# Kernel optimization log

Measured on AMD Instinct MI355X. Metric: run time of the kernel, lower is better.

## Reference

```python
import jax, jax.numpy as jnp
import numpy as np

B, P, K, G_PER, F_IN, H, NECK = 16, 512, 32, 8, 59, 128, 512
N = B * P
E = N * K
G = N // G_PER
EPS = 1e-5


def setup_inputs() -> dict:
    rng = np.random.default_rng(0)
    f32 = lambda a: jnp.asarray(a, jnp.float32)
    x = f32(rng.standard_normal((N, F_IN)))
    pos = f32(rng.standard_normal((N, 3)) * 8.0)
    nrm = rng.standard_normal((N, 3))
    normal = f32(nrm / np.linalg.norm(nrm, axis=1, keepdims=True))
    # synthetic radius-graph edges: K neighbors per node within its own graph, incl. self edge
    nbr = rng.integers(0, P, size=(N, K))
    nbr[:, 0] = np.arange(N) % P  # self edge guarantees every dst segment is non-empty
    starts = np.repeat(np.arange(B) * P, P)
    src = jnp.asarray((starts[:, None] + nbr).reshape(-1), jnp.int32)
    dst = jnp.asarray(np.repeat(np.arange(N), K), jnp.int32)
    # raw (unnormalized but consecutive-run) residue labels, relabeled inside reference
    pool_batch = jnp.asarray(np.repeat(np.arange(G) * 3 + 7, G_PER), jnp.int32)
    mask_t = f32(np.repeat(rng.integers(0, 2, size=G), G_PER))
    def lin(i, o, bias=True):
        w = f32(rng.standard_normal((i, o)) / np.sqrt(i))
        return (w, f32(np.zeros(o))) if bias else w
    lin_w, lin_b = lin(F_IN, H)
    src_w = lin(F_IN, H, bias=False)
    dst_w = lin(F_IN, H, bias=False)
    posnn_w, posnn_b = lin(6, H)
    attnn_w, attnn_b = lin(H, H)
    neck_w, neck_b = lin(H, NECK)
    mlp1_w, mlp1_b = lin(NECK, 256)
    mlp2_w, mlp2_b = lin(256, 1)
    gb = lambda n: (f32(1.0 + 0.1 * rng.standard_normal(n)), f32(0.1 * rng.standard_normal(n)))
    posnn_g, posnn_bb = gb(H)
    attnn_g, attnn_bb = gb(H)
    neck_g, neck_bb = gb(NECK)
    mlp1_g, mlp1_bb = gb(256)
    return dict(x=x, pos=pos, normal=normal, mask_t=mask_t, pool_batch=pool_batch,
                src=src, dst=dst, lin_w=lin_w, lin_b=lin_b, src_w=src_w, dst_w=dst_w,
                posnn_w=posnn_w, posnn_b=posnn_b, posnn_g=posnn_g, posnn_bb=posnn_bb,
                attnn_w=attnn_w, attnn_b=attnn_b, attnn_g=attnn_g, attnn_bb=attnn_bb,
                neck_w=neck_w, neck_b=neck_b, neck_g=neck_g, neck_bb=neck_bb,
                mlp1_w=mlp1_w, mlp1_b=mlp1_b, mlp1_g=mlp1_g, mlp1_bb=mlp1_bb,
                mlp2_w=mlp2_w, mlp2_b=mlp2_b)


def bn_relu(h, g, b):
    # eval-mode BatchNorm1d (running_mean=0, running_var=1) + ReLU; Dropout is identity in eval
    return jax.nn.relu(h * (g / jnp.sqrt(1.0 + EPS)) + b)


def reference(x, pos, normal, mask_t, pool_batch, src, dst,
              lin_w, lin_b, src_w, dst_w,
              posnn_w, posnn_b, posnn_g, posnn_bb,
              attnn_w, attnn_b, attnn_g, attnn_bb,
              neck_w, neck_b, neck_g, neck_bb,
              mlp1_w, mlp1_b, mlp1_g, mlp1_bb,
              mlp2_w, mlp2_b):
    n = x.shape[0]
    # vectorized form of the per-element relabel loop: consecutive runs -> 0..G-1
    chg = jnp.concatenate([jnp.zeros((1,), jnp.int32),
                           (pool_batch[1:] != pool_batch[:-1]).astype(jnp.int32)])
    pb = jnp.cumsum(chg)
    # --- PointTransformerConv (gather -> pos_nn/attn_nn MLPs -> segment softmax -> scatter-add)
    v = x @ lin_w + lin_b                      # value projection [N,H]
    a_src = (x @ src_w)[src]                   # lin_src(x_j)   [E,H]
    a_dst = (x @ dst_w)[dst]                   # lin_dst(x_i)   [E,H]
    rel = jnp.concatenate([pos[dst] - pos[src], normal[dst] - normal[src]], axis=-1)  # [E,6]
    delta = bn_relu(rel @ posnn_w + posnn_b, posnn_g, posnn_bb)                       # [E,H]
    alpha = bn_relu((a_dst - a_src + delta) @ attnn_w + attnn_b, attnn_g, attnn_bb)   # [E,H]
    amax = jax.ops.segment_max(alpha, dst, num_segments=n)
    e = jnp.exp(alpha - amax[dst])
    den = jax.ops.segment_sum(e, dst, num_segments=n)
    attn = e / (den[dst] + 1e-16)              # per-destination softmax over neighbors
    h = jax.ops.segment_sum(attn * (v[src] + delta), dst, num_segments=n)  # [N,H]
    # --- neck, residue max-pool, head
    h = bn_relu(h @ neck_w + neck_b, neck_g, neck_bb)          # [N,512]
    gfeat = jax.ops.segment_max(h, pb, num_segments=G)         # global_max_pool  [G,512]
    gfeat = bn_relu(gfeat @ mlp1_w + mlp1_b, mlp1_g, mlp1_bb)  # [G,256]
    out = gfeat @ mlp2_w + mlp2_b                              # [G,1]
    mask_g = jax.ops.segment_max(mask_t, pb, num_segments=G)   # pooled mask_t
    # original does out[mask_t]; we zero non-selected rows to keep shapes static
    return out * (mask_g == 1.0).astype(out.dtype)[:, None]
```

## Files before the change

### kernel.cpp

```cpp
#include <hip/hip_runtime.h>
#include <hip/hip_bf16.h>
#include <cmath>

#define N_NODES 8192
#define F_INPUT 59
#define H 128
#define K 32
#define NECK 512
#define GPER 8
#define NG 1024
#define EPS_BN 1e-5f
#define LOG2E 1.44269504088896340736f
#define DPITCH 136
#define XPITCH 72
#define PLANE 272

typedef short bf16x8 __attribute__((ext_vector_type(8)));
typedef float f32x16 __attribute__((ext_vector_type(16)));

__device__ __forceinline__ void split_bf(float v, short& hi, short& lo) {
    unsigned u = __float_as_uint(v);
    float hif = __uint_as_float(u & 0xffff0000u);
    hi = (short)(u >> 16);
    lo = (short)(__float_as_uint(v - hif) >> 16);
}
__device__ __forceinline__ short f2bfrn(float f) {
    __hip_bfloat16 b = __float2bfloat16(f);
    return *reinterpret_cast<short*>(&b);
}

__device__ __forceinline__ int bfrag_idx(int k, int c, int k16) {
    int ct = c >> 5, ln = c & 31;
    int s = k >> 4, hf = (k >> 3) & 1, kk = k & 7;
    return ((((ct * k16 + s) * 2 + hf) * 32 + ln) * 8 + kk);
}

__global__ __launch_bounds__(256) void prep_kernel(
    const float* __restrict__ lin_w,
    const float* __restrict__ src_w, const float* __restrict__ dst_w,
    const float* __restrict__ posnn_w,
    const float* __restrict__ attnn_w, const float* __restrict__ attnn_g,
    const float* __restrict__ neck_w,
    short* __restrict__ w3hi, short* __restrict__ w3lo,
    short* __restrict__ pwhi, short* __restrict__ pwlo,
    short* __restrict__ awhi, short* __restrict__ awlo,
    short* __restrict__ nwhi, short* __restrict__ nwlo)
{
    const int b = blockIdx.x;
    if (b < F_INPUT) {
        const int c = threadIdx.x;
        if (c < H) {
            float a1 = 0.f, a2 = 0.f;
            for (int k = 0; k < H; k++) {
                float wa = attnn_w[k * H + c];
                a1 = fmaf(src_w[b * H + k], wa, a1);
                a2 = fmaf(dst_w[b * H + k], wa, a2);
            }
            short hi, lo; int idx;
            split_bf(lin_w[b * H + c], hi, lo);
            idx = bfrag_idx(b, c, 4);       w3hi[idx] = hi; w3lo[idx] = lo;
            split_bf(a1, hi, lo);
            idx = bfrag_idx(b, 128 + c, 4); w3hi[idx] = hi; w3lo[idx] = lo;
            split_bf(a2, hi, lo);
            idx = bfrag_idx(b, 256 + c, 4); w3hi[idx] = hi; w3lo[idx] = lo;
        }
    } else if (b == F_INPUT) {
        for (int t = threadIdx.x; t < 5 * 384; t += 256) {
            int k = F_INPUT + t / 384, c = t % 384;
            int idx = bfrag_idx(k, c, 4);
            w3hi[idx] = 0; w3lo[idx] = 0;
        }
    } else if (b == F_INPUT + 1) {
        for (int idx = threadIdx.x; idx < 2048; idx += 256) {
            int kk = idx & 7; int t = idx >> 3;
            int l2 = t & 31; t >>= 5;
            int hb = t & 1;  t >>= 1;
            int ct = t;
            int k = hb * 8 + kk, c = ct * 32 + l2;
            float wv = (k < 6) ? posnn_w[k * H + c] : 0.f;
            short hi, lo; split_bf(wv, hi, lo);
            pwhi[idx] = hi; pwlo[idx] = lo;
        }
    } else if (b < F_INPUT + 2 + 64) {
        int idx = (b - F_INPUT - 2) * 256 + threadIdx.x;
        int kk = idx & 7; int t = idx >> 3;
        int l2 = t & 31; t >>= 5;
        int hb = t & 1;  t >>= 1;
        int s  = t & 7;  t >>= 3;
        int c = t * 32 + l2, k = s * 16 + hb * 8 + kk;
        float scale = attnn_g[c] * rsqrtf(1.f + EPS_BN) * LOG2E;
        short hi, lo; split_bf(attnn_w[k * H + c] * scale, hi, lo);
        awhi[idx] = hi; awlo[idx] = lo;
    } else {
        int idx = (b - F_INPUT - 2 - 64) * 256 + threadIdx.x;
        int kk = idx & 7; int t = idx >> 3;
        int l2 = t & 31; t >>= 5;
        int hb = t & 1;  t >>= 1;
        int s  = t & 7;  t >>= 3;
        int c = t * 32 + l2, k = s * 16 + hb * 8 + kk;
        short hi, lo; split_bf(neck_w[k * NECK + c], hi, lo);
        nwhi[idx] = hi; nwlo[idx] = lo;
    }
}

__global__ __launch_bounds__(256) void proj_kernel(
    const float* __restrict__ x, const float* __restrict__ lin_b,
    const float* __restrict__ attnn_g, const float* __restrict__ attnn_b,
    const float* __restrict__ attnn_bb,
    const short* __restrict__ w3hi, const short* __restrict__ w3lo,
    float2* __restrict__ vx, float* __restrict__ xdb)
{
    const int n0 = blockIdx.x * 32;
    const int tid = threadIdx.x;
    const int wave = tid >> 6;
    const int lane = tid & 63;
    const int hf = lane >> 5;
    const int ln = lane & 31;

    __shared__ __align__(16) short xhi[32][XPITCH];
    __shared__ __align__(16) short xlo[32][XPITCH];

    for (int idx = tid; idx < 32 * F_INPUT; idx += 256) {
        int n = idx / F_INPUT, k = idx - n * F_INPUT;
        short hi, lo; split_bf(x[n0 * F_INPUT + idx], hi, lo);
        xhi[n][k] = hi; xlo[n][k] = lo;
    }
    if (tid < 32 * 5) {
        int n = tid / 5, k = F_INPUT + tid % 5;
        xhi[n][k] = 0; xlo[n][k] = 0;
    }
    __syncthreads();

    f32x16 acc[3];
    #pragma unroll
    for (int t = 0; t < 3; t++)
        #pragma unroll
        for (int r = 0; r < 16; r++) acc[t][r] = 0.f;

    #pragma unroll
    for (int s = 0; s < 4; s++) {
        bf16x8 ah = *(const bf16x8*)&xhi[ln][s * 16 + hf * 8];
        bf16x8 al = *(const bf16x8*)&xlo[ln][s * 16 + hf * 8];
        #pragma unroll
        for (int t = 0; t < 3; t++) {
            const int ct = wave + 4 * t;
            const int boff = (((ct * 4 + s) * 2 + hf) * 32 + ln) * 8;
            bf16x8 bh = *(const bf16x8*)&w3hi[boff];
            bf16x8 bl = *(const bf16x8*)&w3lo[boff];
            acc[t] = __builtin_amdgcn_mfma_f32_32x32x16_bf16(ah, bl, acc[t], 0, 0, 0);
            acc[t] = __builtin_amdgcn_mfma_f32_32x32x16_bf16(al, bh, acc[t], 0, 0, 0);
            acc[t] = __builtin_amdgcn_mfma_f32_32x32x16_bf16(ah, bh, acc[t], 0, 0, 0);
        }
    }
    const int c = wave * 32 + ln;
    const float lb  = lin_b[c];
    const float s0  = attnn_g[c] * rsqrtf(1.f + EPS_BN);
    const float as_ = s0 * LOG2E;
    const float cbn = fmaf(attnn_b[c], s0, attnn_bb[c]) * LOG2E;
    #pragma unroll
    for (int r = 0; r < 16; r++) {
        int node = n0 + (r & 3) + 8 * (r >> 2) + 4 * hf;
        vx[node * H + c] = make_float2(as_ * acc[1][r], acc[0][r] + lb);
        xdb[node * H + c] = fmaf(acc[2][r], as_, cbn);
    }
}

__global__ __launch_bounds__(256) void edge_kernel(
    const float* __restrict__ pos, const float* __restrict__ normal,
    const int* __restrict__ src,
    const float2* __restrict__ vx, const float* __restrict__ xdb,
    const float* __restrict__ posnn_b, const float* __restrict__ posnn_g,
    const float* __restrict__ posnn_bb,
    const short* __restrict__ pwhi, const short* __restrict__ pwlo,
    const short* __restrict__ awhi, const short* __restrict__ awlo,
    unsigned* __restrict__ h2)
{
    const int i0 = blockIdx.x * 2;
    const int tid = threadIdx.x;
    const int wave = tid >> 6;
    const int lane = tid & 63;
    const int hf = lane >> 5;
    const int ln = lane & 31;

    __shared__ int srcs[2][K];
    __shared__ __align__(16) short dpk[32 * PLANE];

    const int cc = wave * 32 + ln;
    const float ps  = posnn_g[cc] * rsqrtf(1.f + EPS_BN);
    const float pbn = fmaf(posnn_b[cc], ps, posnn_bb[cc]);

    const bf16x8 pbh = *(const bf16x8*)&pwhi[((wave * 2 + hf) * 32 + ln) * 8];
    const bf16x8 pbl = *(const bf16x8*)&pwlo[((wave * 2 + hf) * 32 + ln) * 8];

    bf16x8 rah[2], ral[2];
    #pragma unroll
    for (int n = 0; n < 2; n++)
        #pragma unroll
        for (int k = 0; k < 8; k++) { rah[n][k] = 0; ral[n][k] = 0; }
    if (hf == 0) {
        #pragma unroll
        for (int n = 0; n < 2; n++) {
            const int i = i0 + n;
            int s = src[i * K + ln];
            if (wave == 0) srcs[n][ln] = s * H;
            short h_, l_;
            #pragma unroll
            for (int k = 0; k < 3; k++) {
                split_bf(pos[i * 3 + k] - pos[s * 3 + k], h_, l_);
                rah[n][k] = h_; ral[n][k] = l_;
                split_bf(normal[i * 3 + k] - normal[s * 3 + k], h_, l_);
                rah[n][k + 3] = h_; ral[n][k + 3] = l_;
            }
        }
    }

    const int dbase = ((cc >> 4) * 2 + ((cc >> 3) & 1)) * PLANE + (cc & 7);

    float dreg[2][16];
    #pragma unroll
    for (int n = 0; n < 2; n++) {
        f32x16 da;
        #pragma unroll
        for (int r = 0; r < 16; r++) da[r] = 0.f;
        da = __builtin_amdgcn_mfma_f32_32x32x16_bf16(rah[n], pbl, da, 0, 0, 0);
        da = __builtin_amdgcn_mfma_f32_32x32x16_bf16(ral[n], pbh, da, 0, 0, 0);
        da = __builtin_amdgcn_mfma_f32_32x32x16_bf16(rah[n], pbh, da, 0, 0, 0);
        #pragma unroll
        for (int r = 0; r < 16; r++) {
            int j = (r & 3) + 8 * (r >> 2) + 4 * hf;
            float d = fmaxf(fmaf(da[r], ps, pbn), 0.f);
            dreg[n][r] = d;
            dpk[n * 16 * PLANE + dbase + j * 8] = f2bfrn(d);
        }
    }
    __syncthreads();

    const short* whb = awhi + wave * 8 * 2 * 32 * 8;
    const short* wlb = awlo + wave * 8 * 2 * 32 * 8;

    #pragma unroll
    for (int n = 0; n < 2; n++) {
        const int i = i0 + n;
        f32x16 acc;
        #pragma unroll
        for (int r = 0; r < 16; r++) acc[r] = 0.f;
        #pragma unroll
        for (int s = 0; s < 8; s++) {
            bf16x8 ah = *(const bf16x8*)&dpk[((n * 8 + s) * 2 + hf) * PLANE + ln * 8];
            const int boff = ((s * 2 + hf) * 32 + ln) * 8;
            bf16x8 bh = *(const bf16x8*)&whb[boff];
            bf16x8 bl = *(const bf16x8*)&wlb[boff];
            acc = __builtin_amdgcn_mfma_f32_32x32x16_bf16(ah, bh, acc, 0, 0, 0);
            acc = __builtin_amdgcn_mfma_f32_32x32x16_bf16(ah, bl, acc, 0, 0, 0);
        }

        const float base = xdb[i * H + cc];
        float e[16];
        float den = 0.f;
        #pragma unroll
        for (int r = 0; r < 16; r++) {
            int j = (r & 3) + 8 * (r >> 2) + 4 * hf;
            float2 g = vx[srcs[n][j] + cc];
            float av = fmaxf(acc[r] + base - g.x, 0.f);
            float ev = exp2f(av);
            e[r] = ev;
            den += ev;
            dreg[n][r] += g.y;
        }
        den += __shfl_xor(den, 32, 64);
        const float inv = 1.f / (den + 1e-16f);

        float hsum = 0.f;
        #pragma unroll
        for (int r = 0; r < 16; r++)
            hsum = fmaf(e[r], dreg[n][r], hsum);
        hsum += __shfl_xor(hsum, 32, 64);
        hsum *= inv;
        if (hf == 0) {
            unsigned u = __float_as_uint(hsum);
            unsigned hib = u & 0xffff0000u;
            unsigned lo = __float_as_uint(hsum - __uint_as_float(hib)) >> 16;
            h2[i * H + cc] = (lo << 16) | (u >> 16);
        }
    }
}

__global__ __launch_bounds__(256) void neck_head_kernel(
    const unsigned* __restrict__ h2,
    const short* __restrict__ nwhi, const short* __restrict__ nwlo,
    const float* __restrict__ neck_b, const float* __restrict__ neck_g,
    const float* __restrict__ neck_bb,
    const float* __restrict__ mask_t,
    const float* __restrict__ mlp1_w, const float* __restrict__ mlp1_b,
    const float* __restrict__ mlp1_g, const float* __restrict__ mlp1_bb,
    const float* __restrict__ mlp2_w, const float* __restrict__ mlp2_b,
    float* __restrict__ out)
{
    const int blk = blockIdx.x;
    const int n0 = blk * 32;
    const int tid = threadIdx.x;
    const int wave = tid >> 6;
    const int lane = tid & 63;
    const int hf = lane >> 5;
    const int ln = lane & 31;

    __shared__ __align__(16) short a_hi[32][DPITCH];
    __shared__ __align__(16) short a_lo[32][DPITCH];
    __shared__ float gfeat_l[4][NECK];
    __shared__ float red_l[4][4][256];

    for (int d = tid; d < 32 * H; d += 256) {
        unsigned u = h2[(n0 + (d >> 7)) * H + (d & 127)];
        a_hi[d >> 7][d & 127] = (short)(u & 0xffffu);
        a_lo[d >> 7][d & 127] = (short)(u >> 16);
    }
    __syncthreads();

    f32x16 acc[4];
    #pragma unroll
    for (int t = 0; t < 4; t++)
        #pragma unroll
        for (int r = 0; r < 16; r++) acc[t][r] = 0.f;

    #pragma unroll
    for (int s = 0; s < 8; s++) {
        bf16x8 ah = *(const bf16x8*)&a_hi[ln][s * 16 + hf * 8];
        bf16x8 al = *(const bf16x8*)&a_lo[ln][s * 16 + hf * 8];
        #pragma unroll
        for (int t = 0; t < 4; t++) {
            const int ct = wave * 4 + t;
            const int boff = (((ct * 8 + s) * 2 + hf) * 32 + ln) * 8;
            bf16x8 bh = *(const bf16x8*)&nwhi[boff];
            bf16x8 bl = *(const bf16x8*)&nwlo[boff];
            acc[t] = __builtin_amdgcn_mfma_f32_32x32x16_bf16(ah, bl, acc[t], 0, 0, 0);
            acc[t] = __builtin_amdgcn_mfma_f32_32x32x16_bf16(al, bh, acc[t], 0, 0, 0);
            acc[t] = __builtin_amdgcn_mfma_f32_32x32x16_bf16(ah, bh, acc[t], 0, 0, 0);
        }
    }

    #pragma unroll
    for (int t = 0; t < 4; t++) {
        const int c = wave * 128 + t * 32 + ln;
        const float s  = neck_g[c] * rsqrtf(1.f + EPS_BN);
        const float bnb = fmaf(neck_b[c], s, neck_bb[c]);
        #pragma unroll
        for (int g = 0; g < 4; g++) {
            float m = 0.f;
            #pragma unroll
            for (int q = 0; q < 4; q++)
                m = fmaxf(m, fmaf(acc[t][4 * g + q], s, bnb));
            m = fmaxf(m, __shfl_xor(m, 32, 64));
            if (hf == 0) gfeat_l[g][c] = m;
        }
    }
    __syncthreads();

    const int c4 = lane;
    float ph[4][4];
    #pragma unroll
    for (int g = 0; g < 4; g++)
        #pragma unroll
        for (int mm = 0; mm < 4; mm++) ph[g][mm] = 0.f;

    const int k0 = wave * 128;
    for (int k = 0; k < 128; k += 4) {
        float4 gv[4];
        #pragma unroll
        for (int g = 0; g < 4; g++) gv[g] = *(const float4*)&gfeat_l[g][k0 + k];
        #pragma unroll
        for (int kk = 0; kk < 4; kk++) {
            float w0 = mlp1_w[(k0 + k + kk) * 256 + c4];
            float w1 = mlp1_w[(k0 + k + kk) * 256 + c4 + 64];
            float w2 = mlp1_w[(k0 + k + kk) * 256 + c4 + 128];
            float w3 = mlp1_w[(k0 + k + kk) * 256 + c4 + 192];
            #pragma unroll
            for (int g = 0; g < 4; g++) {
                float gvk = (&gv[g].x)[kk];
                ph[g][0] = fmaf(gvk, w0, ph[g][0]);
                ph[g][1] = fmaf(gvk, w1, ph[g][1]);
                ph[g][2] = fmaf(gvk, w2, ph[g][2]);
                ph[g][3] = fmaf(gvk, w3, ph[g][3]);
            }
        }
    }
    #pragma unroll
    for (int g = 0; g < 4; g++)
        #pragma unroll
        for (int mm = 0; mm < 4; mm++)
            red_l[wave][g][c4 + 64 * mm] = ph[g][mm];
    __syncthreads();

    {
        const int g = wave;
        float part = 0.f;
        #pragma unroll
        for (int mm = 0; mm < 4; mm++) {
            const int c = c4 + 64 * mm;
            float sum = mlp1_b[c] + red_l[0][g][c] + red_l[1][g][c]
                      + red_l[2][g][c] + red_l[3][g][c];
            float s = mlp1_g[c] * rsqrtf(1.f + EPS_BN);
            float val = fmaxf(fmaf(sum, s, mlp1_bb[c]), 0.f);
            part = fmaf(val, mlp2_w[c], part);
        }
        #pragma unroll
        for (int off = 32; off > 0; off >>= 1) part += __shfl_xor(part, off, 64);
        if (lane == 0) {
            const int gg = blk * 4 + g;
            float mm = mask_t[gg * GPER];
            #pragma unroll
            for (int n = 1; n < GPER; n++) mm = fmaxf(mm, mask_t[gg * GPER + n]);
            out[gg] = (mm == 1.0f) ? (part + mlp2_b[0]) : 0.f;
        }
    }
}

extern "C" void kernel_launch(void* const* d_in, const int* in_sizes, int n_in,
                              void* d_out, int out_size, void* d_ws, size_t ws_size,
                              hipStream_t stream)
{
    const float* x        = (const float*)d_in[0];
    const float* pos      = (const float*)d_in[1];
    const float* normal   = (const float*)d_in[2];
    const float* mask_t   = (const float*)d_in[3];
    const int*   src      = (const int*)d_in[5];
    const float* lin_w    = (const float*)d_in[7];
    const float* lin_b    = (const float*)d_in[8];
    const float* src_w    = (const float*)d_in[9];
    const float* dst_w    = (const float*)d_in[10];
    const float* posnn_w  = (const float*)d_in[11];
    const float* posnn_b  = (const float*)d_in[12];
    const float* posnn_g  = (const float*)d_in[13];
    const float* posnn_bb = (const float*)d_in[14];
    const float* attnn_w  = (const float*)d_in[15];
    const float* attnn_b  = (const float*)d_in[16];
    const float* attnn_g  = (const float*)d_in[17];
    const float* attnn_bb = (const float*)d_in[18];
    const float* neck_w   = (const float*)d_in[19];
    const float* neck_b   = (const float*)d_in[20];
    const float* neck_g   = (const float*)d_in[21];
    const float* neck_bb  = (const float*)d_in[22];
    const float* mlp1_w   = (const float*)d_in[23];
    const float* mlp1_b   = (const float*)d_in[24];
    const float* mlp1_g   = (const float*)d_in[25];
    const float* mlp1_bb  = (const float*)d_in[26];
    const float* mlp2_w   = (const float*)d_in[27];
    const float* mlp2_b   = (const float*)d_in[28];

    float* ws = (float*)d_ws;
    float2*   vx   = (float2*)ws;
    float*    xdb  = (float*)(vx + (size_t)N_NODES * H);
    unsigned* h2   = (unsigned*)(xdb + (size_t)N_NODES * H);
    short*    w3hi = (short*)(h2 + (size_t)N_NODES * H);
    short*    w3lo = w3hi + 24576;
    short*    pwhi = w3lo + 24576;
    short*    pwlo = pwhi + 2048;
    short*    awhi = pwlo + 2048;
    short*    awlo = awhi + H * H;
    short*    nwhi = awlo + H * H;
    short*    nwlo = nwhi + H * NECK;

    prep_kernel<<<F_INPUT + 2 + 64 + 256, 256, 0, stream>>>(
        lin_w, src_w, dst_w, posnn_w, attnn_w, attnn_g, neck_w,
        w3hi, w3lo, pwhi, pwlo, awhi, awlo, nwhi, nwlo);
    proj_kernel<<<N_NODES / 32, 256, 0, stream>>>(x, lin_b, attnn_g, attnn_b, attnn_bb,
                                                  w3hi, w3lo, vx, xdb);
    edge_kernel<<<N_NODES / 2, 256, 0, stream>>>(pos, normal, src, vx, xdb,
                                                 posnn_b, posnn_g, posnn_bb,
                                                 pwhi, pwlo, awhi, awlo, h2);
    neck_head_kernel<<<N_NODES / 32, 256, 0, stream>>>(
        h2, nwhi, nwlo, neck_b, neck_g, neck_bb, mask_t,
        mlp1_w, mlp1_b, mlp1_g, mlp1_bb, mlp2_w, mlp2_b, (float*)d_out);
}
```

Baseline: 208.3 us.

## Software-pipeline edge kernel over 8 node pairs with double-buffered LDS

Each edge_kernel block now handles 16 nodes (8 pairs) instead of 2. The pos-MLP delta phase for the next pair is computed into a second LDS buffer while the attention epilogue of the current pair reads the first. This aims to overlap gather latency and MFMA work across pairs and to amortise per-block weight and BN-parameter loads. In exchange, LDS use doubles and register pressure rises, and the grid drops to 512 blocks, which may lower occupancy and load balance.

New measurement: 266.2 us. 1.28x slower.

```diff
diff --git a/kernel.cpp b/kernel.cpp
--- a/kernel.cpp
+++ b/kernel.cpp
@@ -165,6 +165,96 @@
     }
 }
 
+
+#define DELTA_PHASE(PAIR, DPKBUF, SRCSBUF, DREG)                                 \
+{                                                                                \
+    const int ii0 = n_base + (PAIR) * 2;                                         \
+    bf16x8 rah[2], ral[2];                                                       \
+    _Pragma("unroll")                                                            \
+    for (int n = 0; n < 2; n++)                                                  \
+        _Pragma("unroll")                                                        \
+        for (int k = 0; k < 8; k++) { rah[n][k] = 0; ral[n][k] = 0; }            \
+    if (hf == 0) {                                                               \
+        _Pragma("unroll")                                                        \
+        for (int n = 0; n < 2; n++) {                                            \
+            const int i = ii0 + n;                                               \
+            int s = src[i * K + ln];                                             \
+            if (wave == 0) SRCSBUF[n][ln] = s * H;                               \
+            short h_, l_;                                                        \
+            _Pragma("unroll")                                                    \
+            for (int k = 0; k < 3; k++) {                                        \
+                split_bf(pos[i * 3 + k] - pos[s * 3 + k], h_, l_);               \
+                rah[n][k] = h_; ral[n][k] = l_;                                  \
+                split_bf(normal[i * 3 + k] - normal[s * 3 + k], h_, l_);         \
+                rah[n][k + 3] = h_; ral[n][k + 3] = l_;                          \
+            }                                                                    \
+        }                                                                        \
+    }                                                                            \
+    _Pragma("unroll")                                                            \
+    for (int n = 0; n < 2; n++) {                                                \
+        f32x16 da;                                                               \
+        _Pragma("unroll")                                                        \
+        for (int r = 0; r < 16; r++) da[r] = 0.f;                                \
+        da = __builtin_amdgcn_mfma_f32_32x32x16_bf16(rah[n], pbl, da, 0, 0, 0);  \
+        da = __builtin_amdgcn_mfma_f32_32x32x16_bf16(ral[n], pbh, da, 0, 0, 0);  \
+        da = __builtin_amdgcn_mfma_f32_32x32x16_bf16(rah[n], pbh, da, 0, 0, 0);  \
+        _Pragma("unroll")                                                        \
+        for (int r = 0; r < 16; r++) {                                           \
+            int j = (r & 3) + 8 * (r >> 2) + 4 * hf;                             \
+            float d = fmaxf(fmaf(da[r], ps, pbn), 0.f);                          \
+            DREG[n][r] = d;                                                      \
+            DPKBUF[n * 16 * PLANE + dbase + j * 8] = f2bfrn(d);                  \
+        }                                                                        \
+    }                                                                            \
+}
+
+#define EPILOGUE_PHASE(PAIR, DPKBUF, SRCSBUF, DREG)                              \
+{                                                                                \
+    _Pragma("unroll")                                                            \
+    for (int n = 0; n < 2; n++) {                                                \
+        const int i = n_base + (PAIR) * 2 + n;                                   \
+        f32x16 acc;                                                              \
+        _Pragma("unroll")                                                        \
+        for (int r = 0; r < 16; r++) acc[r] = 0.f;                               \
+        _Pragma("unroll")                                                        \
+        for (int s = 0; s < 8; s++) {                                            \
+            bf16x8 ah = *(const bf16x8*)&DPKBUF[((n * 8 + s) * 2 + hf) * PLANE + ln * 8]; \
+            const int boff = ((s * 2 + hf) * 32 + ln) * 8;                       \
+            bf16x8 bh = *(const bf16x8*)&whb[boff];                              \
+            bf16x8 bl = *(const bf16x8*)&wlb[boff];                              \
+            acc = __builtin_amdgcn_mfma_f32_32x32x16_bf16(ah, bh, acc, 0, 0, 0); \
+            acc = __builtin_amdgcn_mfma_f32_32x32x16_bf16(ah, bl, acc, 0, 0, 0); \
+        }                                                                        \
+        const float base = xdb[i * H + cc];                                      \
+        float e[16];                                                             \
+        float den = 0.f;                                                         \
+        _Pragma("unroll")                                                        \
+        for (int r = 0; r < 16; r++) {                                           \
+            int j = (r & 3) + 8 * (r >> 2) + 4 * hf;                             \
+            float2 g = vx[SRCSBUF[n][j] + cc];                                   \
+            float av = fmaxf(acc[r] + base - g.x, 0.f);                          \
+            float ev = exp2f(av);                                                \
+            e[r] = ev;                                                           \
+            den += ev;                                                           \
+            DREG[n][r] += g.y;                                                   \
+        }                                                                        \
+        den += __shfl_xor(den, 32, 64);                                          \
+        const float inv = 1.f / (den + 1e-16f);                                  \
+        float hsum = 0.f;                                                        \
+        _Pragma("unroll")                                                        \
+        for (int r = 0; r < 16; r++)                                             \
+            hsum = fmaf(e[r], DREG[n][r], hsum);                                 \
+        hsum += __shfl_xor(hsum, 32, 64);                                        \
+        hsum *= inv;                                                             \
+        if (hf == 0) {                                                           \
+            unsigned u = __float_as_uint(hsum);                                  \
+            unsigned hib = u & 0xffff0000u;                                      \
+            unsigned lo = __float_as_uint(hsum - __uint_as_float(hib)) >> 16;    \
+            h2[i * H + cc] = (lo << 16) | (u >> 16);                             \
+        }                                                                        \
+    }                                                                            \
+}
+
 __global__ __launch_bounds__(256) void edge_kernel(
     const float* __restrict__ pos, const float* __restrict__ normal,
     const int* __restrict__ src,
@@ -175,15 +265,16 @@
     const short* __restrict__ awhi, const short* __restrict__ awlo,
     unsigned* __restrict__ h2)
 {
-    const int i0 = blockIdx.x * 2;
+    const int n_base = blockIdx.x * 16;
     const int tid = threadIdx.x;
     const int wave = tid >> 6;
     const int lane = tid & 63;
     const int hf = lane >> 5;
     const int ln = lane & 31;
 
-    __shared__ int srcs[2][K];
-    __shared__ __align__(16) short dpk[32 * PLANE];
+    __shared__ int srcs0[2][K], srcs1[2][K];
+    __shared__ __align__(16) short dpk0[32 * PLANE];
+    __shared__ __align__(16) short dpk1[32 * PLANE];
 
     const int cc = wave * 32 + ln;
     const float ps  = posnn_g[cc] * rsqrtf(1.f + EPS_BN);
@@ -192,96 +283,23 @@
     const bf16x8 pbh = *(const bf16x8*)&pwhi[((wave * 2 + hf) * 32 + ln) * 8];
     const bf16x8 pbl = *(const bf16x8*)&pwlo[((wave * 2 + hf) * 32 + ln) * 8];
 
-    bf16x8 rah[2], ral[2];
-    #pragma unroll
-    for (int n = 0; n < 2; n++)
-        #pragma unroll
-        for (int k = 0; k < 8; k++) { rah[n][k] = 0; ral[n][k] = 0; }
-    if (hf == 0) {
-        #pragma unroll
-        for (int n = 0; n < 2; n++) {
-            const int i = i0 + n;
-            int s = src[i * K + ln];
-            if (wave == 0) srcs[n][ln] = s * H;
-            short h_, l_;
-            #pragma unroll
-            for (int k = 0; k < 3; k++) {
-                split_bf(pos[i * 3 + k] - pos[s * 3 + k], h_, l_);
-                rah[n][k] = h_; ral[n][k] = l_;
-                split_bf(normal[i * 3 + k] - normal[s * 3 + k], h_, l_);
-                rah[n][k + 3] = h_; ral[n][k + 3] = l_;
-            }
-        }
-    }
-
     const int dbase = ((cc >> 4) * 2 + ((cc >> 3) & 1)) * PLANE + (cc & 7);
-
-    float dreg[2][16];
-    #pragma unroll
-    for (int n = 0; n < 2; n++) {
-        f32x16 da;
-        #pragma unroll
-        for (int r = 0; r < 16; r++) da[r] = 0.f;
-        da = __builtin_amdgcn_mfma_f32_32x32x16_bf16(rah[n], pbl, da, 0, 0, 0);
-        da = __builtin_amdgcn_mfma_f32_32x32x16_bf16(ral[n], pbh, da, 0, 0, 0);
-        da = __builtin_amdgcn_mfma_f32_32x32x16_bf16(rah[n], pbh, da, 0, 0, 0);
-        #pragma unroll
-        for (int r = 0; r < 16; r++) {
-            int j = (r & 3) + 8 * (r >> 2) + 4 * hf;
-            float d = fmaxf(fmaf(da[r], ps, pbn), 0.f);
-            dreg[n][r] = d;
-            dpk[n * 16 * PLANE + dbase + j * 8] = f2bfrn(d);
-        }
-    }
-    __syncthreads();
 
     const short* whb = awhi + wave * 8 * 2 * 32 * 8;
     const short* wlb = awlo + wave * 8 * 2 * 32 * 8;
 
-    #pragma unroll
-    for (int n = 0; n < 2; n++) {
-        const int i = i0 + n;
-        f32x16 acc;
-        #pragma unroll
-        for (int r = 0; r < 16; r++) acc[r] = 0.f;
-        #pragma unroll
-        for (int s = 0; s < 8; s++) {
-            bf16x8 ah = *(const bf16x8*)&dpk[((n * 8 + s) * 2 + hf) * PLANE + ln * 8];
-            const int boff = ((s * 2 + hf) * 32 + ln) * 8;
-            bf16x8 bh = *(const bf16x8*)&whb[boff];
-            bf16x8 bl = *(const bf16x8*)&wlb[boff];
-            acc = __builtin_amdgcn_mfma_f32_32x32x16_bf16(ah, bh, acc, 0, 0, 0);
-            acc = __builtin_amdgcn_mfma_f32_32x32x16_bf16(ah, bl, acc, 0, 0, 0);
-        }
-
-        const float base = xdb[i * H + cc];
-        float e[16];
-        float den = 0.f;
-        #pragma unroll
-        for (int r = 0; r < 16; r++) {
-            int j = (r & 3) + 8 * (r >> 2) + 4 * hf;
-            float2 g = vx[srcs[n][j] + cc];
-            float av = fmaxf(acc[r] + base - g.x, 0.f);
-            float ev = exp2f(av);
-            e[r] = ev;
-            den += ev;
-            dreg[n][r] += g.y;
-        }
-        den += __shfl_xor(den, 32, 64);
-        const float inv = 1.f / (den + 1e-16f);
-
-        float hsum = 0.f;
-        #pragma unroll
-        for (int r = 0; r < 16; r++)
-            hsum = fmaf(e[r], dreg[n][r], hsum);
-        hsum += __shfl_xor(hsum, 32, 64);
-        hsum *= inv;
-        if (hf == 0) {
-            unsigned u = __float_as_uint(hsum);
-            unsigned hib = u & 0xffff0000u;
-            unsigned lo = __float_as_uint(hsum - __uint_as_float(hib)) >> 16;
-            h2[i * H + cc] = (lo << 16) | (u >> 16);
-        }
+    float dregA[2][16], dregB[2][16];
+
+    DELTA_PHASE(0, dpk0, srcs0, dregA)
+
+    #pragma unroll
+    for (int p = 0; p < 8; p += 2) {
+        __syncthreads();
+        if (p + 1 < 8) DELTA_PHASE(p + 1, dpk1, srcs1, dregB)
+        EPILOGUE_PHASE(p, dpk0, srcs0, dregA)
+        __syncthreads();
+        if (p + 2 < 8) DELTA_PHASE(p + 2, dpk0, srcs0, dregA)
+        if (p + 1 < 8) EPILOGUE_PHASE(p + 1, dpk1, srcs1, dregB)
     }
 }
 
@@ -464,9 +482,9 @@
         w3hi, w3lo, pwhi, pwlo, awhi, awlo, nwhi, nwlo);
     proj_kernel<<<N_NODES / 32, 256, 0, stream>>>(x, lin_b, attnn_g, attnn_b, attnn_bb,
                                                   w3hi, w3lo, vx, xdb);
-    edge_kernel<<<N_NODES / 2, 256, 0, stream>>>(pos, normal, src, vx, xdb,
-                                                 posnn_b, posnn_g, posnn_bb,
-                                                 pwhi, pwlo, awhi, awlo, h2);
+    edge_kernel<<<N_NODES / 16, 256, 0, stream>>>(pos, normal, src, vx, xdb,
+                                                  posnn_b, posnn_g, posnn_bb,
+                                                  pwhi, pwlo, awhi, awlo, h2);
     neck_head_kernel<<<N_NODES / 32, 256, 0, stream>>>(
         h2, nwhi, nwlo, neck_b, neck_g, neck_bb, mask_t,
         mlp1_w, mlp1_b, mlp1_g, mlp1_bb, mlp2_w, mlp2_b, (float*)d_out);
```
